# Kernel tuning notes

Hardware: AMD Instinct MI355X
Metric: run time of the kernel (lower is better)

## Reference

```python
import jax, jax.numpy as jnp
import numpy as np

B, N, C = 4, 2048, 768
H = 6  # 3 obj heads + 3 pose heads (forced by the chained matmul shapes)


def setup_inputs() -> dict:
    key = jax.random.key(0)
    k1, k2, k3 = jax.random.split(key, 3)
    x = jax.random.normal(k1, (B, N, C), dtype=jnp.float32)
    w_qkv = jax.random.normal(k2, (3 * C, C), dtype=jnp.float32) * (C ** -0.5)
    w_proj = jax.random.normal(k3, (C, C // 2), dtype=jnp.float32) * ((C // 2) ** -0.5)
    b_proj = jnp.zeros((C,), dtype=jnp.float32)
    return {"x": x, "w_qkv": w_qkv, "w_proj": w_proj, "b_proj": b_proj, "num_heads": H}


def reference(x, w_qkv, w_proj, b_proj, num_heads):
    b, n, c = x.shape
    hd = c // num_heads
    scale = hd ** -0.5
    # qkv projection -> [3, B, H, N, hd]
    qkv = (x @ w_qkv.T).reshape(b, n, 3, num_heads, hd)
    qkv = jnp.transpose(qkv, (2, 0, 3, 1, 4))
    q, k, v = qkv[0], qkv[1], qkv[2]
    # head split: first 3 heads -> obj (sigmoid), last 3 -> pose (softmax)
    attn_obj = jax.nn.sigmoid(jnp.einsum('bhqd,bhkd->bhqk', q[:, 0:3], k[:, 0:3]) * scale)
    attn_pose = jax.nn.softmax(jnp.einsum('bhqd,bhkd->bhqk', q[:, 3:], k[:, 3:]) * scale, axis=-1)
    # chained matmuls: (attn_pose @ (attn_obj @ v_pose))  -> [B, 3, N, hd]
    ctx = jnp.einsum('bhqk,bhkd->bhqd', attn_obj, v[:, 3:])
    ctx = jnp.einsum('bhqk,bhkd->bhqd', attn_pose, ctx)
    out = jnp.transpose(ctx, (0, 2, 1, 3)).reshape(b, n, c // 2)
    out = out @ w_proj.T + b_proj
    return out, attn_obj
```

## Files before the change

kernel.cpp:

```cpp
#include <hip/hip_runtime.h>

typedef _Float16 half8 __attribute__((ext_vector_type(8)));
typedef _Float16 half4v __attribute__((ext_vector_type(4)));
typedef float f32x4 __attribute__((ext_vector_type(4)));
typedef float f32x16 __attribute__((ext_vector_type(16)));

#define MFMA16(a, b, c) __builtin_amdgcn_mfma_f32_16x16x32_f16((a), (b), (c), 0, 0, 0)
#define MFMA32(a, b, c) __builtin_amdgcn_mfma_f32_32x32x16_f16((a), (b), (c), 0, 0, 0)
#define FENCE() __builtin_amdgcn_sched_barrier(0)
#define BAR() __builtin_amdgcn_s_barrier()

__device__ __forceinline__ void gl_lds16(const void* g, void* l) {
  __builtin_amdgcn_global_load_lds(
      (const __attribute__((address_space(1))) unsigned int*)g,
      (__attribute__((address_space(3))) unsigned int*)l, 16, 0, 0);
}

__device__ __forceinline__ unsigned pkh2(float a, float b) {
  unsigned lo = (unsigned)__builtin_bit_cast(unsigned short, (_Float16)a);
  unsigned hf = (unsigned)__builtin_bit_cast(unsigned short, (_Float16)b);
  return lo | (hf << 16);
}

__global__ __launch_bounds__(256) void k_cvt_all(const float* __restrict__ x,
                                                 const float* __restrict__ wq,
                                                 const float* __restrict__ wp,
                                                 _Float16* __restrict__ xb,
                                                 _Float16* __restrict__ wqb,
                                                 _Float16* __restrict__ wpb) {
  int i = blockIdx.x * 256 + threadIdx.x;
  const float4* src;
  half4v* dst;
  int j;
  if (i < 1572864) { src = (const float4*)x; dst = (half4v*)xb; j = i; }
  else if (i < 1572864 + 442368) { src = (const float4*)wq; dst = (half4v*)wqb; j = i - 1572864; }
  else if (i < 2088960) { src = (const float4*)wp; dst = (half4v*)wpb; j = i - 2015232; }
  else return;
  float4 v = src[j];
  half4v h;
  h[0] = (_Float16)v.x; h[1] = (_Float16)v.y;
  h[2] = (_Float16)v.z; h[3] = (_Float16)v.w;
  dst[j] = h;
}

__global__ __launch_bounds__(256) void k_qkv(const _Float16* __restrict__ A,
                                             const _Float16* __restrict__ Bt,
                                             _Float16* __restrict__ Qw,
                                             _Float16* __restrict__ Kw,
                                             _Float16* __restrict__ Vtw) {
  __shared__ _Float16 As[2][128 * 32];
  __shared__ _Float16 Bs[2][128 * 32];
  const int tid = threadIdx.x;
  const int w = tid >> 6, l = tid & 63;
  const int wr = w >> 1, wc = w & 1;
  const int bid0 = blockIdx.x;
  const int bid = (bid0 & 7) * 144 + (bid0 >> 3);
  const int tm = bid / 18, tn = bid % 18;
  const int m0 = tm * 128, n0 = tn * 128;

  auto stage = [&](int it, int dst) {
    int k0 = it * 32;
#pragma unroll
    for (int r = 0; r < 2; ++r) {
      int seg = r * 256 + tid;
      int row = seg >> 2, cs = seg & 3;
      gl_lds16(A + (size_t)(m0 + row) * 768 + k0 + cs * 8, (char*)As[dst] + (r * 256 + w * 64) * 16);
      gl_lds16(Bt + (size_t)(n0 + row) * 768 + k0 + cs * 8, (char*)Bs[dst] + (r * 256 + w * 64) * 16);
    }
  };

  f32x4 acc[4][4] = {};
  stage(0, 0);
  asm volatile("s_waitcnt vmcnt(0)" ::: "memory");
  BAR();
  for (int it = 0; it < 24; ++it) {
    const int cur = it & 1;
    stage(it < 23 ? it + 1 : 23, cur ^ 1);
    asm volatile("s_waitcnt vmcnt(4)" ::: "memory");
    FENCE();
    BAR();
    FENCE();
#pragma unroll
    for (int m = 0; m < 4; ++m) {
      half8 av = *(const half8*)&As[cur][(wr * 64 + m * 16 + (l & 15)) * 32 + (l >> 4) * 8];
#pragma unroll
      for (int n = 0; n < 4; ++n) {
        half8 bv = *(const half8*)&Bs[cur][(wc * 64 + n * 16 + (l & 15)) * 32 + (l >> 4) * 8];
        acc[m][n] = MFMA16(av, bv, acc[m][n]);
      }
    }
    FENCE();
    BAR();
  }
  asm volatile("s_waitcnt vmcnt(0)" ::: "memory");

  const float scale = 0.08838834764831845f;
#pragma unroll
  for (int m = 0; m < 4; ++m) {
    int gmb = m0 + wr * 64 + m * 16 + ((l >> 4) << 2);
#pragma unroll
    for (int n = 0; n < 4; ++n) {
      int gn0 = n0 + wc * 64 + n * 16;
      int t = gn0 / 768, rem = gn0 % 768;
      int h = rem >> 7, d = (rem & 127) + (l & 15);
      if (t == 2) {
        int bB = gmb >> 11, ntok0 = gmb & 2047;
        half4v hv;
#pragma unroll
        for (int j = 0; j < 4; ++j) hv[j] = (_Float16)acc[m][n][j];
        *(half4v*)&Vtw[((size_t)(bB * 6 + h) * 128 + d) * 2048 + ntok0] = hv;
      } else {
#pragma unroll
        for (int j = 0; j < 4; ++j) {
          int gm = gmb + j;
          int b = gm >> 11, ntok = gm & 2047;
          float v = acc[m][n][j];
          if (t == 0)
            Qw[((size_t)(b * 6 + h) * 2048 + ntok) * 128 + d] = (_Float16)(v * scale);
          else
            Kw[((size_t)(b * 6 + h) * 2048 + ntok) * 128 + d] = (_Float16)v;
        }
      }
    }
  }
}

__global__ __launch_bounds__(256, 2) void k_obj(const _Float16* __restrict__ Qw,
                                                const _Float16* __restrict__ Kw,
                                                const _Float16* __restrict__ Vtw,
                                                float* __restrict__ attn,
                                                _Float16* __restrict__ c1t) {
  __shared__ _Float16 Ks[2][64 * 128];
  __shared__ _Float16 Vs[128 * 64];
  __shared__ float Ts[4][1024];
  const int tid = threadIdx.x, w = tid >> 6, l = tid & 63;
  const int wr = w >> 1, wc = w & 1, hi = l >> 5, q = l & 31;
  const int bid0 = blockIdx.x;
  const int bid = (bid0 & 7) * 48 + (bid0 >> 3);
  const int b = bid / 96, rem = bid % 96, h = rem / 32, qb = rem % 32;
  const _Float16* Qg = Qw + ((size_t)(b * 6 + h) * 2048 + qb * 64 + wr * 32) * 128;
  const _Float16* Kg = Kw + ((size_t)(b * 6 + h) * 2048) * 128;
  const _Float16* Vg = Vtw + ((size_t)(b * 6 + h + 3) * 128) * 2048;
  float* attng = attn + ((size_t)(b * 3 + h) * 2048 + qb * 64) * 2048;

  auto stageK = [&](int t, int dstb) {
#pragma unroll
    for (int r = 0; r < 4; ++r) {
      int seg = r * 256 + tid;
      int row = seg >> 4, cs = (seg & 15) ^ (row & 7);
      gl_lds16(Kg + (size_t)(t * 64 + row) * 128 + cs * 8,
               (char*)Ks[dstb] + (r * 256 + w * 64) * 16);
    }
  };
  auto stageV = [&](int t) {
#pragma unroll
    for (int r = 0; r < 4; ++r) {
      int seg = r * 256 + tid;
      int row = seg >> 3, cs = (seg & 7) ^ (row & 7);
      gl_lds16(Vg + (size_t)row * 2048 + t * 64 + cs * 8,
               (char*)Vs + (r * 256 + w * 64) * 16);
    }
  };

  half8 qreg[8];
#pragma unroll
  for (int s = 0; s < 8; ++s)
    qreg[s] = *(const half8*)&Qg[(size_t)q * 128 + s * 16 + hi * 8];
  stageK(0, 0);

  f32x16 acc[4] = {};
  for (int kt = 0; kt < 32; ++kt) {
    const int cur = kt & 1, nxt = cur ^ 1;
    stageV(kt);
    stageK((kt + 1) & 31, nxt);
    asm volatile("s_waitcnt vmcnt(8)" ::: "memory");
    FENCE(); BAR(); FENCE();
    f32x16 p = {};
    const int krow = wc * 32 + q;
    __builtin_amdgcn_s_setprio(1);
#pragma unroll
    for (int s = 0; s < 8; ++s) {
      int chunk = (s * 2 + hi) ^ (krow & 7);
      half8 av = *(const half8*)&Ks[cur][krow * 128 + chunk * 8];
      p = MFMA32(av, qreg[s], p);
    }
    __builtin_amdgcn_s_setprio(0);
#pragma unroll
    for (int r = 0; r < 16; ++r) p[r] = 1.0f / (1.0f + __expf(-p[r]));
    union { unsigned uu[4]; half8 v; } bf0, bf1;
    {
      unsigned pk01 = pkh2(p[0], p[1]), pk23 = pkh2(p[2], p[3]);
      unsigned pk45 = pkh2(p[4], p[5]), pk67 = pkh2(p[6], p[7]);
      unsigned x = hi ? pk01 : pk45, y = hi ? pk23 : pk67;
      unsigned xsw = (unsigned)__shfl_xor((int)x, 32);
      unsigned ysw = (unsigned)__shfl_xor((int)y, 32);
      bf0.uu[0] = hi ? xsw : pk01; bf0.uu[1] = hi ? ysw : pk23;
      bf0.uu[2] = hi ? pk45 : xsw; bf0.uu[3] = hi ? pk67 : ysw;
    }
    {
      unsigned pk01 = pkh2(p[8], p[9]), pk23 = pkh2(p[10], p[11]);
      unsigned pk45 = pkh2(p[12], p[13]), pk67 = pkh2(p[14], p[15]);
      unsigned x = hi ? pk01 : pk45, y = hi ? pk23 : pk67;
      unsigned xsw = (unsigned)__shfl_xor((int)x, 32);
      unsigned ysw = (unsigned)__shfl_xor((int)y, 32);
      bf1.uu[0] = hi ? xsw : pk01; bf1.uu[1] = hi ? ysw : pk23;
      bf1.uu[2] = hi ? pk45 : xsw; bf1.uu[3] = hi ? pk67 : ysw;
    }
    asm volatile("s_waitcnt vmcnt(4)" ::: "memory");
    FENCE(); BAR(); FENCE();
    __builtin_amdgcn_s_setprio(1);
#pragma unroll
    for (int ks = 0; ks < 2; ++ks) {
#pragma unroll
      for (int dt = 0; dt < 4; ++dt) {
        int vrow = dt * 32 + q;
        int chunk = (wc * 4 + ks * 2 + hi) ^ (vrow & 7);
        half8 av = *(const half8*)&Vs[vrow * 64 + chunk * 8];
        acc[dt] = MFMA32(av, ks ? bf1.v : bf0.v, acc[dt]);
      }
    }
    __builtin_amdgcn_s_setprio(0);
    {
      float* T = Ts[w];
#pragma unroll
      for (int r = 0; r < 16; ++r) {
        int kv = (r & 3) + 8 * (r >> 2) + 4 * hi;
        T[q * 32 + (kv ^ ((q & 7) << 2))] = p[r];
      }
#pragma unroll
      for (int i = 0; i < 4; ++i) {
        int qr = (l >> 3) + 8 * i;
        int kvq = (l & 7) * 4;
        f32x4 v4 = *(const f32x4*)&T[qr * 32 + (kvq ^ ((qr & 7) << 2))];
        *(f32x4*)&attng[(size_t)(wr * 32 + qr) * 2048 + kt * 64 + wc * 32 + kvq] = v4;
      }
    }
    FENCE();
    BAR();
  }
  __syncthreads();
  float* mb = (float*)Ks;
  if (wc == 1) {
#pragma unroll
    for (int dt = 0; dt < 4; ++dt)
#pragma unroll
      for (int r = 0; r < 16; ++r) {
        int d = dt * 32 + (r & 3) + 8 * (r >> 2) + 4 * hi;
        mb[(wr * 128 + d) * 32 + q] = acc[dt][r];
      }
  }
  __syncthreads();
  if (wc == 0) {
    _Float16* cg = c1t + (size_t)(b * 3 + h) * 128 * 2048;
    int n = qb * 64 + wr * 32 + q;
#pragma unroll
    for (int dt = 0; dt < 4; ++dt)
#pragma unroll
      for (int r = 0; r < 16; ++r) {
        int d = dt * 32 + (r & 3) + 8 * (r >> 2) + 4 * hi;
        cg[(size_t)d * 2048 + n] = (_Float16)(acc[dt][r] + mb[(wr * 128 + d) * 32 + q]);
      }
  }
}

__global__ __launch_bounds__(256, 3) void k_pose(const _Float16* __restrict__ Qw,
                                                 const _Float16* __restrict__ Kw,
                                                 const _Float16* __restrict__ c1t,
                                                 _Float16* __restrict__ c2) {
  __shared__ _Float16 Ks[2][64 * 128];
  __shared__ _Float16 Cs[128 * 64];
  __shared__ float lbuf[64];
  const int tid = threadIdx.x, w = tid >> 6, l = tid & 63;
  const int wr = w >> 1, wc = w & 1, hi = l >> 5, q = l & 31;
  const int bid0 = blockIdx.x;
  const int bid = (bid0 & 7) * 48 + (bid0 >> 3);
  const int b = bid / 96, rem = bid % 96, h = rem / 32, qb = rem % 32;
  const _Float16* Qg = Qw + ((size_t)(b * 6 + h + 3) * 2048 + qb * 64 + wr * 32) * 128;
  const _Float16* Kg = Kw + ((size_t)(b * 6 + h + 3) * 2048) * 128;
  const _Float16* Cg = c1t + ((size_t)(b * 3 + h) * 128) * 2048;

  auto stageK = [&](int t, int dstb) {
#pragma unroll
    for (int r = 0; r < 4; ++r) {
      int seg = r * 256 + tid;
      int row = seg >> 4, cs = (seg & 15) ^ (row & 7);
      gl_lds16(Kg + (size_t)(t * 64 + row) * 128 + cs * 8,
               (char*)Ks[dstb] + (r * 256 + w * 64) * 16);
    }
  };
  auto stageC = [&](int t) {
#pragma unroll
    for (int r = 0; r < 4; ++r) {
      int seg = r * 256 + tid;
      int row = seg >> 3, cs = (seg & 7) ^ (row & 7);
      gl_lds16(Cg + (size_t)row * 2048 + t * 64 + cs * 8,
               (char*)Cs + (r * 256 + w * 64) * 16);
    }
  };

  half8 qreg[8];
#pragma unroll
  for (int s = 0; s < 8; ++s)
    qreg[s] = *(const half8*)&Qg[(size_t)q * 128 + s * 16 + hi * 8];
  stageK(0, 0);

  f32x16 acc[4] = {};
  float lsum = 0.f;
  for (int kt = 0; kt < 32; ++kt) {
    const int cur = kt & 1, nxt = cur ^ 1;
    stageC(kt);
    stageK((kt + 1) & 31, nxt);
    asm volatile("s_waitcnt vmcnt(8)" ::: "memory");
    FENCE(); BAR(); FENCE();
    f32x16 p = {};
    const int krow = wc * 32 + q;
    __builtin_amdgcn_s_setprio(1);
#pragma unroll
    for (int s = 0; s < 8; ++s) {
      int chunk = (s * 2 + hi) ^ (krow & 7);
      half8 av = *(const half8*)&Ks[cur][krow * 128 + chunk * 8];
      p = MFMA32(av, qreg[s], p);
    }
    __builtin_amdgcn_s_setprio(0);
#pragma unroll
    for (int r = 0; r < 16; ++r) {
      p[r] = __expf(p[r]);
      lsum += p[r];
    }
    union { unsigned uu[4]; half8 v; } bf0, bf1;
    {
      unsigned pk01 = pkh2(p[0], p[1]), pk23 = pkh2(p[2], p[3]);
      unsigned pk45 = pkh2(p[4], p[5]), pk67 = pkh2(p[6], p[7]);
      unsigned x = hi ? pk01 : pk45, y = hi ? pk23 : pk67;
      unsigned xsw = (unsigned)__shfl_xor((int)x, 32);
      unsigned ysw = (unsigned)__shfl_xor((int)y, 32);
      bf0.uu[0] = hi ? xsw : pk01; bf0.uu[1] = hi ? ysw : pk23;
      bf0.uu[2] = hi ? pk45 : xsw; bf0.uu[3] = hi ? pk67 : ysw;
    }
    {
      unsigned pk01 = pkh2(p[8], p[9]), pk23 = pkh2(p[10], p[11]);
      unsigned pk45 = pkh2(p[12], p[13]), pk67 = pkh2(p[14], p[15]);
      unsigned x = hi ? pk01 : pk45, y = hi ? pk23 : pk67;
      unsigned xsw = (unsigned)__shfl_xor((int)x, 32);
      unsigned ysw = (unsigned)__shfl_xor((int)y, 32);
      bf1.uu[0] = hi ? xsw : pk01; bf1.uu[1] = hi ? ysw : pk23;
      bf1.uu[2] = hi ? pk45 : xsw; bf1.uu[3] = hi ? pk67 : ysw;
    }
    asm volatile("s_waitcnt vmcnt(4)" ::: "memory");
    FENCE(); BAR(); FENCE();
    __builtin_amdgcn_s_setprio(1);
#pragma unroll
    for (int ks = 0; ks < 2; ++ks) {
#pragma unroll
      for (int dt = 0; dt < 4; ++dt) {
        int vrow = dt * 32 + q;
        int chunk = (wc * 4 + ks * 2 + hi) ^ (vrow & 7);
        half8 av = *(const half8*)&Cs[vrow * 64 + chunk * 8];
        acc[dt] = MFMA32(av, ks ? bf1.v : bf0.v, acc[dt]);
      }
    }
    __builtin_amdgcn_s_setprio(0);
    FENCE();
    BAR();
  }
  __syncthreads();
  float lsum2 = lsum + (float)__shfl_xor(lsum, 32);
  float* mb = (float*)Ks;
  _Float16* ob = (_Float16*)Cs;
  if (wc == 1) {
#pragma unroll
    for (int dt = 0; dt < 4; ++dt)
#pragma unroll
      for (int r = 0; r < 16; ++r) {
        int d = dt * 32 + (r & 3) + 8 * (r >> 2) + 4 * hi;
        mb[(wr * 128 + d) * 32 + q] = acc[dt][r];
      }
    if (l < 32) lbuf[wr * 32 + q] = lsum2;
  }
  __syncthreads();
  if (wc == 0) {
    float inv = 1.0f / (lsum2 + lbuf[wr * 32 + q]);
    int qbl = wr * 32 + q;
#pragma unroll
    for (int dt = 0; dt < 4; ++dt)
#pragma unroll
      for (int g = 0; g < 4; ++g) {
        int d0 = dt * 32 + 8 * g + 4 * hi;
        float v0 = (acc[dt][4 * g + 0] + mb[(wr * 128 + d0 + 0) * 32 + q]) * inv;
        float v1 = (acc[dt][4 * g + 1] + mb[(wr * 128 + d0 + 1) * 32 + q]) * inv;
        float v2 = (acc[dt][4 * g + 2] + mb[(wr * 128 + d0 + 2) * 32 + q]) * inv;
        float v3 = (acc[dt][4 * g + 3] + mb[(wr * 128 + d0 + 3) * 32 + q]) * inv;
        union { unsigned u[2]; half4v v; } hv;
        hv.u[0] = pkh2(v0, v1);
        hv.u[1] = pkh2(v2, v3);
        int c8 = (d0 >> 2) ^ ((qbl & 7) << 2);
        *(half4v*)&ob[qbl * 128 + c8 * 4] = hv.v;
      }
  }
  __syncthreads();
  {
    _Float16* cg = c2 + ((size_t)b * 2048 + qb * 64) * 384 + h * 128;
    int qbl = tid >> 2;
#pragma unroll
    for (int j = 0; j < 4; ++j) {
      int ii = (tid & 3) + j * 4;
      int c8 = (ii * 2) ^ ((qbl & 7) << 2);
      half8 v = *(const half8*)&ob[qbl * 128 + c8 * 4];
      *(half8*)&cg[(size_t)qbl * 384 + ii * 8] = v;
    }
  }
}

__global__ __launch_bounds__(256) void k_proj(const _Float16* __restrict__ A,
                                              const _Float16* __restrict__ Bt,
                                              const float* __restrict__ bias,
                                              float* __restrict__ out) {
  __shared__ _Float16 As[2][128 * 32];
  __shared__ _Float16 Bs[2][128 * 32];
  const int tid = threadIdx.x;
  const int w = tid >> 6, l = tid & 63;
  const int wr = w >> 1, wc = w & 1;
  const int bid0 = blockIdx.x;
  const int bid = (bid0 & 7) * 48 + (bid0 >> 3);
  const int tm = bid / 6, tn = bid % 6;
  const int m0 = tm * 128, n0 = tn * 128;

  auto stage = [&](int it, int dst) {
    int k0 = it * 32;
#pragma unroll
    for (int r = 0; r < 2; ++r) {
      int seg = r * 256 + tid;
      int row = seg >> 2, cs = seg & 3;
      gl_lds16(A + (size_t)(m0 + row) * 384 + k0 + cs * 8, (char*)As[dst] + (r * 256 + w * 64) * 16);
      gl_lds16(Bt + (size_t)(n0 + row) * 384 + k0 + cs * 8, (char*)Bs[dst] + (r * 256 + w * 64) * 16);
    }
  };

  f32x4 acc[4][4] = {};
  stage(0, 0);
  asm volatile("s_waitcnt vmcnt(0)" ::: "memory");
  BAR();
  for (int it = 0; it < 12; ++it) {
    const int cur = it & 1;
    stage(it < 11 ? it + 1 : 11, cur ^ 1);
    asm volatile("s_waitcnt vmcnt(4)" ::: "memory");
    FENCE();
    BAR();
    FENCE();
#pragma unroll
    for (int m = 0; m < 4; ++m) {
      half8 av = *(const half8*)&As[cur][(wr * 64 + m * 16 + (l & 15)) * 32 + (l >> 4) * 8];
#pragma unroll
      for (int n = 0; n < 4; ++n) {
        half8 bv = *(const half8*)&Bs[cur][(wc * 64 + n * 16 + (l & 15)) * 32 + (l >> 4) * 8];
        acc[m][n] = MFMA16(av, bv, acc[m][n]);
      }
    }
    FENCE();
    BAR();
  }
  asm volatile("s_waitcnt vmcnt(0)" ::: "memory");

#pragma unroll
  for (int m = 0; m < 4; ++m) {
    int gmb = m0 + wr * 64 + m * 16 + ((l >> 4) << 2);
#pragma unroll
    for (int n = 0; n < 4; ++n) {
      int gn = n0 + wc * 64 + n * 16 + (l & 15);
      float bv = bias[gn];
#pragma unroll
      for (int j = 0; j < 4; ++j) {
        int gm = gmb + j;
        out[(size_t)gm * 768 + gn] = acc[m][n][j] + bv;
      }
    }
  }
}

extern "C" void kernel_launch(void* const* d_in, const int* in_sizes, int n_in,
                              void* d_out, int out_size, void* d_ws, size_t ws_size,
                              hipStream_t stream) {
  const float* x = (const float*)d_in[0];
  const float* wqkv = (const float*)d_in[1];
  const float* wproj = (const float*)d_in[2];
  const float* bproj = (const float*)d_in[3];

  _Float16* xb = (_Float16*)d_ws;
  _Float16* wqkvb = xb + 6291456;
  _Float16* wprojb = wqkvb + 1769472;
  _Float16* Qw = wprojb + 294912;
  _Float16* Kw = Qw + 6291456;
  _Float16* Vtw = Kw + 6291456;
  _Float16* c1t = Vtw + 6291456;
  _Float16* c2 = c1t + 3145728;

  float* out = (float*)d_out;
  float* attn = out + 6291456;

  k_cvt_all<<<8160, 256, 0, stream>>>(x, wqkv, wproj, xb, wqkvb, wprojb);
  k_qkv<<<1152, 256, 0, stream>>>(xb, wqkvb, Qw, Kw, Vtw);
  k_obj<<<384, 256, 0, stream>>>(Qw, Kw, Vtw, attn, c1t);
  k_pose<<<384, 256, 0, stream>>>(Qw, Kw, c1t, c2);
  k_proj<<<384, 256, 0, stream>>>(c2, wprojb, bproj, out);
}
```

Baseline: 216.1 us.

## Double-buffer V/C tiles, deepen GEMM K-tiles with swizzle, split MFMA chains

The QKV and projection GEMMs now stage 64-wide K tiles with an XOR-swizzled LDS layout, which halves the loop trip count and the number of barriers. The obj and pose attention kernels now double-buffer the V/C tiles together with the K tiles in one prefetch. This removes the second mid-iteration wait and barrier. The QK^T MFMA chain is split into two independent accumulators to shorten the dependency chain, and the attn store is moved before the PV MFMAs. The cost is more LDS per block, and k_pose drops from 3 to 2 blocks per SM in its occupancy hint.

```diff
diff --git a/kernel.cpp b/kernel.cpp
--- a/kernel.cpp
+++ b/kernel.cpp
@@ -48,22 +48,22 @@
                                              _Float16* __restrict__ Qw,
                                              _Float16* __restrict__ Kw,
                                              _Float16* __restrict__ Vtw) {
-  __shared__ _Float16 As[2][128 * 32];
-  __shared__ _Float16 Bs[2][128 * 32];
+  __shared__ _Float16 As[2][128 * 64];
+  __shared__ _Float16 Bs[2][128 * 64];
   const int tid = threadIdx.x;
   const int w = tid >> 6, l = tid & 63;
-  const int wr = w >> 1, wc = w & 1;
+  const int wr = w >> 1, wc = w & 1, hi = l >> 4;
   const int bid0 = blockIdx.x;
   const int bid = (bid0 & 7) * 144 + (bid0 >> 3);
   const int tm = bid / 18, tn = bid % 18;
   const int m0 = tm * 128, n0 = tn * 128;
 
   auto stage = [&](int it, int dst) {
-    int k0 = it * 32;
-#pragma unroll
-    for (int r = 0; r < 2; ++r) {
+    int k0 = it * 64;
+#pragma unroll
+    for (int r = 0; r < 4; ++r) {
       int seg = r * 256 + tid;
-      int row = seg >> 2, cs = seg & 3;
+      int row = seg >> 3, cs = (seg & 7) ^ (row & 7);
       gl_lds16(A + (size_t)(m0 + row) * 768 + k0 + cs * 8, (char*)As[dst] + (r * 256 + w * 64) * 16);
       gl_lds16(Bt + (size_t)(n0 + row) * 768 + k0 + cs * 8, (char*)Bs[dst] + (r * 256 + w * 64) * 16);
     }
@@ -73,20 +73,25 @@
   stage(0, 0);
   asm volatile("s_waitcnt vmcnt(0)" ::: "memory");
   BAR();
-  for (int it = 0; it < 24; ++it) {
+  for (int it = 0; it < 12; ++it) {
     const int cur = it & 1;
-    stage(it < 23 ? it + 1 : 23, cur ^ 1);
-    asm volatile("s_waitcnt vmcnt(4)" ::: "memory");
+    stage(it < 11 ? it + 1 : 11, cur ^ 1);
+    asm volatile("s_waitcnt vmcnt(8)" ::: "memory");
     FENCE();
     BAR();
     FENCE();
 #pragma unroll
-    for (int m = 0; m < 4; ++m) {
-      half8 av = *(const half8*)&As[cur][(wr * 64 + m * 16 + (l & 15)) * 32 + (l >> 4) * 8];
-#pragma unroll
-      for (int n = 0; n < 4; ++n) {
-        half8 bv = *(const half8*)&Bs[cur][(wc * 64 + n * 16 + (l & 15)) * 32 + (l >> 4) * 8];
-        acc[m][n] = MFMA16(av, bv, acc[m][n]);
+    for (int ks = 0; ks < 2; ++ks) {
+#pragma unroll
+      for (int m = 0; m < 4; ++m) {
+        int rowa = wr * 64 + m * 16 + (l & 15);
+        half8 av = *(const half8*)&As[cur][rowa * 64 + (((ks * 4 + hi) ^ (rowa & 7)) * 8)];
+#pragma unroll
+        for (int n = 0; n < 4; ++n) {
+          int rowb = wc * 64 + n * 16 + (l & 15);
+          half8 bv = *(const half8*)&Bs[cur][rowb * 64 + (((ks * 4 + hi) ^ (rowb & 7)) * 8)];
+          acc[m][n] = MFMA16(av, bv, acc[m][n]);
+        }
       }
     }
     FENCE();
@@ -131,7 +136,7 @@
                                                 float* __restrict__ attn,
                                                 _Float16* __restrict__ c1t) {
   __shared__ _Float16 Ks[2][64 * 128];
-  __shared__ _Float16 Vs[128 * 64];
+  __shared__ _Float16 Vs[2][128 * 64];
   __shared__ float Ts[4][1024];
   const int tid = threadIdx.x, w = tid >> 6, l = tid & 63;
   const int wr = w >> 1, wc = w & 1, hi = l >> 5, q = l & 31;
@@ -143,22 +148,16 @@
   const _Float16* Vg = Vtw + ((size_t)(b * 6 + h + 3) * 128) * 2048;
   float* attng = attn + ((size_t)(b * 3 + h) * 2048 + qb * 64) * 2048;
 
-  auto stageK = [&](int t, int dstb) {
+  auto stagePair = [&](int t, int dstb) {
 #pragma unroll
     for (int r = 0; r < 4; ++r) {
       int seg = r * 256 + tid;
       int row = seg >> 4, cs = (seg & 15) ^ (row & 7);
       gl_lds16(Kg + (size_t)(t * 64 + row) * 128 + cs * 8,
                (char*)Ks[dstb] + (r * 256 + w * 64) * 16);
-    }
-  };
-  auto stageV = [&](int t) {
-#pragma unroll
-    for (int r = 0; r < 4; ++r) {
-      int seg = r * 256 + tid;
-      int row = seg >> 3, cs = (seg & 7) ^ (row & 7);
-      gl_lds16(Vg + (size_t)row * 2048 + t * 64 + cs * 8,
-               (char*)Vs + (r * 256 + w * 64) * 16);
+      int rowv = seg >> 3, csv = (seg & 7) ^ (rowv & 7);
+      gl_lds16(Vg + (size_t)rowv * 2048 + t * 64 + csv * 8,
+               (char*)Vs[dstb] + (r * 256 + w * 64) * 16);
     }
   };
 
@@ -166,27 +165,47 @@
 #pragma unroll
   for (int s = 0; s < 8; ++s)
     qreg[s] = *(const half8*)&Qg[(size_t)q * 128 + s * 16 + hi * 8];
-  stageK(0, 0);
+  stagePair(0, 0);
+  asm volatile("s_waitcnt vmcnt(0)" ::: "memory");
+  BAR();
 
   f32x16 acc[4] = {};
   for (int kt = 0; kt < 32; ++kt) {
-    const int cur = kt & 1, nxt = cur ^ 1;
-    stageV(kt);
-    stageK((kt + 1) & 31, nxt);
-    asm volatile("s_waitcnt vmcnt(8)" ::: "memory");
+    const int cur = kt & 1;
+    stagePair((kt + 1) & 31, cur ^ 1);
+    asm volatile("s_waitcnt vmcnt(12)" ::: "memory");
     FENCE(); BAR(); FENCE();
-    f32x16 p = {};
+    f32x16 p0 = {}, p1 = {};
     const int krow = wc * 32 + q;
     __builtin_amdgcn_s_setprio(1);
 #pragma unroll
-    for (int s = 0; s < 8; ++s) {
-      int chunk = (s * 2 + hi) ^ (krow & 7);
-      half8 av = *(const half8*)&Ks[cur][krow * 128 + chunk * 8];
-      p = MFMA32(av, qreg[s], p);
+    for (int s = 0; s < 4; ++s) {
+      int c0 = (s * 2 + hi) ^ (krow & 7);
+      half8 a0 = *(const half8*)&Ks[cur][krow * 128 + c0 * 8];
+      p0 = MFMA32(a0, qreg[s], p0);
+      int c1 = ((s + 4) * 2 + hi) ^ (krow & 7);
+      half8 a1 = *(const half8*)&Ks[cur][krow * 128 + c1 * 8];
+      p1 = MFMA32(a1, qreg[s + 4], p1);
     }
     __builtin_amdgcn_s_setprio(0);
+    f32x16 p = p0 + p1;
 #pragma unroll
     for (int r = 0; r < 16; ++r) p[r] = 1.0f / (1.0f + __expf(-p[r]));
+    {
+      float* T = Ts[w];
+#pragma unroll
+      for (int r = 0; r < 16; ++r) {
+        int kv = (r & 3) + 8 * (r >> 2) + 4 * hi;
+        T[q * 32 + (kv ^ ((q & 7) << 2))] = p[r];
+      }
+#pragma unroll
+      for (int i = 0; i < 4; ++i) {
+        int qr = (l >> 3) + 8 * i;
+        int kvq = (l & 7) * 4;
+        f32x4 v4 = *(const f32x4*)&T[qr * 32 + (kvq ^ ((qr & 7) << 2))];
+        *(f32x4*)&attng[(size_t)(wr * 32 + qr) * 2048 + kt * 64 + wc * 32 + kvq] = v4;
+      }
+    }
     union { unsigned uu[4]; half8 v; } bf0, bf1;
     {
       unsigned pk01 = pkh2(p[0], p[1]), pk23 = pkh2(p[2], p[3]);
@@ -206,8 +225,6 @@
       bf1.uu[0] = hi ? xsw : pk01; bf1.uu[1] = hi ? ysw : pk23;
       bf1.uu[2] = hi ? pk45 : xsw; bf1.uu[3] = hi ? pk67 : ysw;
     }
-    asm volatile("s_waitcnt vmcnt(4)" ::: "memory");
-    FENCE(); BAR(); FENCE();
     __builtin_amdgcn_s_setprio(1);
 #pragma unroll
     for (int ks = 0; ks < 2; ++ks) {
@@ -215,26 +232,11 @@
       for (int dt = 0; dt < 4; ++dt) {
         int vrow = dt * 32 + q;
         int chunk = (wc * 4 + ks * 2 + hi) ^ (vrow & 7);
-        half8 av = *(const half8*)&Vs[vrow * 64 + chunk * 8];
+        half8 av = *(const half8*)&Vs[cur][vrow * 64 + chunk * 8];
         acc[dt] = MFMA32(av, ks ? bf1.v : bf0.v, acc[dt]);
       }
     }
     __builtin_amdgcn_s_setprio(0);
-    {
-      float* T = Ts[w];
-#pragma unroll
-      for (int r = 0; r < 16; ++r) {
-        int kv = (r & 3) + 8 * (r >> 2) + 4 * hi;
-        T[q * 32 + (kv ^ ((q & 7) << 2))] = p[r];
-      }
-#pragma unroll
-      for (int i = 0; i < 4; ++i) {
-        int qr = (l >> 3) + 8 * i;
-        int kvq = (l & 7) * 4;
-        f32x4 v4 = *(const f32x4*)&T[qr * 32 + (kvq ^ ((qr & 7) << 2))];
-        *(f32x4*)&attng[(size_t)(wr * 32 + qr) * 2048 + kt * 64 + wc * 32 + kvq] = v4;
-      }
-    }
     FENCE();
     BAR();
   }
@@ -263,12 +265,12 @@
   }
 }
 
-__global__ __launch_bounds__(256, 3) void k_pose(const _Float16* __restrict__ Qw,
+__global__ __launch_bounds__(256, 2) void k_pose(const _Float16* __restrict__ Qw,
                                                  const _Float16* __restrict__ Kw,
                                                  const _Float16* __restrict__ c1t,
                                                  _Float16* __restrict__ c2) {
   __shared__ _Float16 Ks[2][64 * 128];
-  __shared__ _Float16 Cs[128 * 64];
+  __shared__ _Float16 Cs[2][128 * 64];
   __shared__ float lbuf[64];
   const int tid = threadIdx.x, w = tid >> 6, l = tid & 63;
   const int wr = w >> 1, wc = w & 1, hi = l >> 5, q = l & 31;
@@ -279,22 +281,16 @@
   const _Float16* Kg = Kw + ((size_t)(b * 6 + h + 3) * 2048) * 128;
   const _Float16* Cg = c1t + ((size_t)(b * 3 + h) * 128) * 2048;
 
-  auto stageK = [&](int t, int dstb) {
+  auto stagePair = [&](int t, int dstb) {
 #pragma unroll
     for (int r = 0; r < 4; ++r) {
       int seg = r * 256 + tid;
       int row = seg >> 4, cs = (seg & 15) ^ (row & 7);
       gl_lds16(Kg + (size_t)(t * 64 + row) * 128 + cs * 8,
                (char*)Ks[dstb] + (r * 256 + w * 64) * 16);
-    }
-  };
-  auto stageC = [&](int t) {
-#pragma unroll
-    for (int r = 0; r < 4; ++r) {
-      int seg = r * 256 + tid;
-      int row = seg >> 3, cs = (seg & 7) ^ (row & 7);
-      gl_lds16(Cg + (size_t)row * 2048 + t * 64 + cs * 8,
-               (char*)Cs + (r * 256 + w * 64) * 16);
+      int rowv = seg >> 3, csv = (seg & 7) ^ (rowv & 7);
+      gl_lds16(Cg + (size_t)rowv * 2048 + t * 64 + csv * 8,
+               (char*)Cs[dstb] + (r * 256 + w * 64) * 16);
     }
   };
 
@@ -302,26 +298,31 @@
 #pragma unroll
   for (int s = 0; s < 8; ++s)
     qreg[s] = *(const half8*)&Qg[(size_t)q * 128 + s * 16 + hi * 8];
-  stageK(0, 0);
+  stagePair(0, 0);
+  asm volatile("s_waitcnt vmcnt(0)" ::: "memory");
+  BAR();
 
   f32x16 acc[4] = {};
   float lsum = 0.f;
   for (int kt = 0; kt < 32; ++kt) {
-    const int cur = kt & 1, nxt = cur ^ 1;
-    stageC(kt);
-    stageK((kt + 1) & 31, nxt);
+    const int cur = kt & 1;
+    stagePair((kt + 1) & 31, cur ^ 1);
     asm volatile("s_waitcnt vmcnt(8)" ::: "memory");
     FENCE(); BAR(); FENCE();
-    f32x16 p = {};
+    f32x16 p0 = {}, p1 = {};
     const int krow = wc * 32 + q;
     __builtin_amdgcn_s_setprio(1);
 #pragma unroll
-    for (int s = 0; s < 8; ++s) {
-      int chunk = (s * 2 + hi) ^ (krow & 7);
-      half8 av = *(const half8*)&Ks[cur][krow * 128 + chunk * 8];
-      p = MFMA32(av, qreg[s], p);
+    for (int s = 0; s < 4; ++s) {
+      int c0 = (s * 2 + hi) ^ (krow & 7);
+      half8 a0 = *(const half8*)&Ks[cur][krow * 128 + c0 * 8];
+      p0 = MFMA32(a0, qreg[s], p0);
+      int c1 = ((s + 4) * 2 + hi) ^ (krow & 7);
+      half8 a1 = *(const half8*)&Ks[cur][krow * 128 + c1 * 8];
+      p1 = MFMA32(a1, qreg[s + 4], p1);
     }
     __builtin_amdgcn_s_setprio(0);
+    f32x16 p = p0 + p1;
 #pragma unroll
     for (int r = 0; r < 16; ++r) {
       p[r] = __expf(p[r]);
@@ -346,8 +347,6 @@
       bf1.uu[0] = hi ? xsw : pk01; bf1.uu[1] = hi ? ysw : pk23;
       bf1.uu[2] = hi ? pk45 : xsw; bf1.uu[3] = hi ? pk67 : ysw;
     }
-    asm volatile("s_waitcnt vmcnt(4)" ::: "memory");
-    FENCE(); BAR(); FENCE();
     __builtin_amdgcn_s_setprio(1);
 #pragma unroll
     for (int ks = 0; ks < 2; ++ks) {
@@ -355,7 +354,7 @@
       for (int dt = 0; dt < 4; ++dt) {
         int vrow = dt * 32 + q;
         int chunk = (wc * 4 + ks * 2 + hi) ^ (vrow & 7);
-        half8 av = *(const half8*)&Cs[vrow * 64 + chunk * 8];
+        half8 av = *(const half8*)&Cs[cur][vrow * 64 + chunk * 8];
         acc[dt] = MFMA32(av, ks ? bf1.v : bf0.v, acc[dt]);
       }
     }
@@ -415,22 +414,22 @@
                                               const _Float16* __restrict__ Bt,
                                               const float* __restrict__ bias,
                                               float* __restrict__ out) {
-  __shared__ _Float16 As[2][128 * 32];
-  __shared__ _Float16 Bs[2][128 * 32];
+  __shared__ _Float16 As[2][128 * 64];
+  __shared__ _Float16 Bs[2][128 * 64];
   const int tid = threadIdx.x;
   const int w = tid >> 6, l = tid & 63;
-  const int wr = w >> 1, wc = w & 1;
+  const int wr = w >> 1, wc = w & 1, hi = l >> 4;
   const int bid0 = blockIdx.x;
   const int bid = (bid0 & 7) * 48 + (bid0 >> 3);
   const int tm = bid / 6, tn = bid % 6;
   const int m0 = tm * 128, n0 = tn * 128;
 
   auto stage = [&](int it, int dst) {
-    int k0 = it * 32;
-#pragma unroll
-    for (int r = 0; r < 2; ++r) {
+    int k0 = it * 64;
+#pragma unroll
+    for (int r = 0; r < 4; ++r) {
       int seg = r * 256 + tid;
-      int row = seg >> 2, cs = seg & 3;
+      int row = seg >> 3, cs = (seg & 7) ^ (row & 7);
       gl_lds16(A + (size_t)(m0 + row) * 384 + k0 + cs * 8, (char*)As[dst] + (r * 256 + w * 64) * 16);
       gl_lds16(Bt + (size_t)(n0 + row) * 384 + k0 + cs * 8, (char*)Bs[dst] + (r * 256 + w * 64) * 16);
     }
@@ -440,20 +439,25 @@
   stage(0, 0);
   asm volatile("s_waitcnt vmcnt(0)" ::: "memory");
   BAR();
-  for (int it = 0; it < 12; ++it) {
+  for (int it = 0; it < 6; ++it) {
     const int cur = it & 1;
-    stage(it < 11 ? it + 1 : 11, cur ^ 1);
-    asm volatile("s_waitcnt vmcnt(4)" ::: "memory");
+    stage(it < 5 ? it + 1 : 5, cur ^ 1);
+    asm volatile("s_waitcnt vmcnt(8)" ::: "memory");
     FENCE();
     BAR();
     FENCE();
 #pragma unroll
-    for (int m = 0; m < 4; ++m) {
-      half8 av = *(const half8*)&As[cur][(wr * 64 + m * 16 + (l & 15)) * 32 + (l >> 4) * 8];
-#pragma unroll
-      for (int n = 0; n < 4; ++n) {
-        half8 bv = *(const half8*)&Bs[cur][(wc * 64 + n * 16 + (l & 15)) * 32 + (l >> 4) * 8];
-        acc[m][n] = MFMA16(av, bv, acc[m][n]);
+    for (int ks = 0; ks < 2; ++ks) {
+#pragma unroll
+      for (int m = 0; m < 4; ++m) {
+        int rowa = wr * 64 + m * 16 + (l & 15);
+        half8 av = *(const half8*)&As[cur][rowa * 64 + (((ks * 4 + hi) ^ (rowa & 7)) * 8)];
+#pragma unroll
+        for (int n = 0; n < 4; ++n) {
+          int rowb = wc * 64 + n * 16 + (l & 15);
+          half8 bv = *(const half8*)&Bs[cur][rowb * 64 + (((ks * 4 + hi) ^ (rowb & 7)) * 8)];
+          acc[m][n] = MFMA16(av, bv, acc[m][n]);
+        }
       }
     }
     FENCE();
```

New measurement: 213.7 us. About the same (-1.1%).
